# Kernel tuning notes

Hardware: AMD Instinct MI355X
Metric: run time of the kernel (lower is better)

## Reference

```python
import jax, jax.numpy as jnp
import numpy as np


def setup_inputs() -> dict:
    key = jax.random.key(0)
    ks = jax.random.split(key, 5)
    B, T, D, L = 4, 8192, 1024, 128
    X = jax.random.normal(ks[0], (B, T, D), dtype=jnp.float32)
    attention_mask = jnp.ones((B, T), dtype=jnp.float32)
    sd_dl = 1.0 / np.sqrt(D)  # lecun_normal fan_in = D
    Wk = jax.random.normal(ks[1], (D, L), dtype=jnp.float32) * sd_dl
    Wq = jax.random.normal(ks[2], (D, L), dtype=jnp.float32) * sd_dl
    Wv = jax.random.normal(ks[3], (D, D), dtype=jnp.float32) * sd_dl
    o_proj = jax.random.normal(ks[4], (D, D), dtype=jnp.float32) * sd_dl
    return {"X": X, "attention_mask": attention_mask, "Wk": Wk, "Wq": Wq,
            "Wv": Wv, "o_proj": o_proj, "n_heads": 16}


def reference(X, attention_mask, Wk, Wq, Wv, o_proj, n_heads):
    B, T, D = X.shape
    H = n_heads
    # Projections, laid out time-major as in the original: (T, B, H, *)
    V = jnp.einsum('DM,BTD->TBM', Wv, X).reshape(T, B, H, -1)   # (T,B,H,d)
    Q = jnp.einsum('DL,BTD->TBL', Wq, X).reshape(T, B, H, -1)   # (T,B,H,l)
    K = jnp.einsum('DL,BTD->TBL', Wk, X).reshape(T, B, H, -1)   # (T,B,H,l)
    m = attention_mask.T[:, :, None, None]                       # (T,B,1,1)
    V = V * m
    Qs = jax.nn.softmax(Q, axis=-1)
    maxi = jnp.max(K, axis=0, keepdims=True)                     # global max over T
    K = jnp.exp(K - maxi) * m
    Kv = jnp.einsum('tbhl,tbhd->bhld', K, V)                     # global KV state
    Ksum = K.sum(axis=0)                                         # (B,H,l)
    Kv = Kv / Ksum[..., None]
    y = jnp.einsum('tbhl,bhld->bthd', Qs, Kv).reshape(B, T, D)
    return y @ o_proj
```

## Files before the change

kernel.cpp:

```cpp
#include <hip/hip_runtime.h>
#include <hip/hip_bf16.h>

typedef unsigned short u16;
typedef unsigned int   u32;

typedef __attribute__((ext_vector_type(8))) short short8;
typedef __attribute__((ext_vector_type(4))) float f32x4;

typedef const __attribute__((address_space(1))) void g_void;
typedef __attribute__((address_space(3))) void l_void;

__device__ __forceinline__ float bf2f(u16 u) {
    u32 x = ((u32)u) << 16;
    return __builtin_bit_cast(float, x);
}
__device__ __forceinline__ u16 f2bf(float f) {
    u32 u = __builtin_bit_cast(u32, f);
    u32 r = (u + 0x7FFFu + ((u >> 16) & 1u)) >> 16;
    return (u16)r;
}
__device__ __forceinline__ u32 pack2(float a, float b) {
    return (u32)f2bf(a) | ((u32)f2bf(b) << 16);
}

__global__ void detect_kernel(const u16* __restrict__ X, int* __restrict__ flags) {
    __shared__ int cnt[256];
    int c = 0;
    for (int i = threadIdx.x; i < 16384; i += 256) {
        u16 v = X[i];
        int e = (v >> 7) & 0xFF;
        c += (e >= 104 && e <= 140) ? 1 : 0;
    }
    cnt[threadIdx.x] = c;
    __syncthreads();
    for (int s = 128; s > 0; s >>= 1) {
        if (threadIdx.x < s) cnt[threadIdx.x] += cnt[threadIdx.x + s];
        __syncthreads();
    }
    if (threadIdx.x == 0) {
        flags[0] = (cnt[0] < 14746) ? 1 : 0;
        flags[1] = 0;
    }
}

__global__ __launch_bounds__(256) void convert_x(const float* __restrict__ Xf,
                                                 u16* __restrict__ XC,
                                                 const int* __restrict__ flags, int n) {
    if (flags[0] == 0) return;
    int i = (blockIdx.x * 256 + threadIdx.x) * 8;
    if (i >= n) return;
    float4 a = *(const float4*)(Xf + i);
    float4 b = *(const float4*)(Xf + i + 4);
    uint4 o;
    o.x = pack2(a.x, a.y); o.y = pack2(a.z, a.w);
    o.z = pack2(b.x, b.y); o.w = pack2(b.z, b.w);
    *(uint4*)(XC + i) = o;
}

__global__ void convert_mask(const void* __restrict__ m, float* __restrict__ MC,
                             const int* __restrict__ flags, int n) {
    int i = blockIdx.x * 256 + threadIdx.x;
    if (i >= n) return;
    MC[i] = flags[0] ? ((const float*)m)[i] : bf2f(((const u16*)m)[i]);
}

__global__ __launch_bounds__(256) void gemm_bt(
    const u16* __restrict__ A0, const u16* __restrict__ A1, int lda,
    const u16* __restrict__ Bt, int ldb,
    void* __restrict__ C, int ldc,
    int Mtiles, int K,
    const int* __restrict__ aselp, const int* __restrict__ ofp) {
    __shared__ char smem[16384];

    const u16* A = aselp[0] ? A1 : A0;

    const int tid = threadIdx.x;
    const int w = tid >> 6, lane = tid & 63;
    const int mt = blockIdx.x % Mtiles;
    const int nt = blockIdx.x / Mtiles;
    const int m0 = mt << 7, n0 = nt << 7;
    const int wm = w >> 1, wn = w & 1;

    f32x4 acc[4][4] = {};

    const int rr = w * 16 + (lane >> 2);
    const int cg = (lane & 3) ^ ((lane >> 3) & 3);

    const u16* gA0 = A + (m0 + rr) * lda + cg * 8;
    const u16* gA1 = A + (m0 + rr + 64) * lda + cg * 8;
    const u16* gB0 = Bt + (n0 + rr) * ldb + cg * 8;
    const u16* gB1 = Bt + (n0 + rr + 64) * ldb + cg * 8;

    char* lA0 = smem + w * 1024 + lane * 16;
    char* lA1 = smem + 4096 + w * 1024 + lane * 16;
    char* lB0 = smem + 8192 + w * 1024 + lane * 16;
    char* lB1 = smem + 12288 + w * 1024 + lane * 16;

    const int fr_a = (wm << 6) + (lane & 15);
    const int fr_b = (wn << 6) + (lane & 15);
    const int sl = (lane >> 4) ^ ((lane >> 1) & 3);
    const char* pA = smem + fr_a * 64 + sl * 16;
    const char* pB = smem + 8192 + fr_b * 64 + sl * 16;

    for (int kt = 0; kt < K; kt += 32) {
        __builtin_amdgcn_global_load_lds((g_void*)(gA0 + kt), (l_void*)lA0, 16, 0, 0);
        __builtin_amdgcn_global_load_lds((g_void*)(gA1 + kt), (l_void*)lA1, 16, 0, 0);
        __builtin_amdgcn_global_load_lds((g_void*)(gB0 + kt), (l_void*)lB0, 16, 0, 0);
        __builtin_amdgcn_global_load_lds((g_void*)(gB1 + kt), (l_void*)lB1, 16, 0, 0);
        __syncthreads();
        short8 af[4], bfv[4];
#pragma unroll
        for (int i = 0; i < 4; ++i) {
            af[i]  = *(const short8*)(pA + i * 1024);
            bfv[i] = *(const short8*)(pB + i * 1024);
        }
#pragma unroll
        for (int mi = 0; mi < 4; ++mi) {
#pragma unroll
            for (int ni = 0; ni < 4; ++ni) {
                acc[mi][ni] = __builtin_amdgcn_mfma_f32_16x16x32_bf16(
                    af[mi], bfv[ni], acc[mi][ni], 0, 0, 0);
            }
        }
        __syncthreads();
    }

    const int out_fp32 = ofp[0];
    float* fb = (float*)smem;
    const int lrow = tid >> 3, cgp = tid & 7;
#pragma unroll
    for (int mi = 0; mi < 4; ++mi) {
#pragma unroll
        for (int ni = 0; ni < 4; ++ni) {
#pragma unroll
            for (int r = 0; r < 4; ++r) {
                int lr = wm * 16 + ((lane >> 4) << 2) + r;
                int lc = wn * 64 + ni * 16 + (lane & 15);
                fb[lr * 128 + lc] = acc[mi][ni][r];
            }
        }
        __syncthreads();
        int grow = (lrow < 16) ? (mi * 16 + lrow) : (48 + mi * 16 + lrow);
        const float* srcp = fb + lrow * 128 + cgp * 16;
        if (out_fp32) {
            float4* dst = (float4*)((float*)C + (size_t)(m0 + grow) * ldc + n0 + cgp * 16);
            dst[0] = make_float4(srcp[0], srcp[1], srcp[2], srcp[3]);
            dst[1] = make_float4(srcp[4], srcp[5], srcp[6], srcp[7]);
            dst[2] = make_float4(srcp[8], srcp[9], srcp[10], srcp[11]);
            dst[3] = make_float4(srcp[12], srcp[13], srcp[14], srcp[15]);
        } else {
            u32 o0 = pack2(srcp[0], srcp[1]);
            u32 o1 = pack2(srcp[2], srcp[3]);
            u32 o2 = pack2(srcp[4], srcp[5]);
            u32 o3 = pack2(srcp[6], srcp[7]);
            u32 o4 = pack2(srcp[8], srcp[9]);
            u32 o5 = pack2(srcp[10], srcp[11]);
            u32 o6 = pack2(srcp[12], srcp[13]);
            u32 o7 = pack2(srcp[14], srcp[15]);
            uint4* dst = (uint4*)((u16*)C + (size_t)(m0 + grow) * ldc + n0 + cgp * 16);
            dst[0] = make_uint4(o0, o1, o2, o3);
            dst[1] = make_uint4(o4, o5, o6, o7);
        }
        __syncthreads();
    }
}

__device__ __forceinline__ u16 rd_elem(const void* s, int idx, int fp32) {
    return fp32 ? f2bf(((const float*)s)[idx]) : ((const u16*)s)[idx];
}

__global__ void transpose_k(const void* __restrict__ Wq, const void* __restrict__ Wk,
                            const void* __restrict__ Wv, const void* __restrict__ Op,
                            u16* __restrict__ W1T, u16* __restrict__ OpT,
                            const int* __restrict__ flags) {
    int fp32 = flags[0];
    int id = blockIdx.x;
    const void* src; u16* dst; int Nc, mid;
    if (id < 128)       { src = Wq; dst = W1T;               Nc = 128;  mid = id; }
    else if (id < 256)  { src = Wk; dst = W1T + 128 * 1024;  Nc = 128;  mid = id - 128; }
    else if (id < 1280) { src = Wv; dst = W1T + 256 * 1024;  Nc = 1024; mid = id - 256; }
    else                { src = Op; dst = OpT;               Nc = 1024; mid = id - 1280; }
    int kt = mid & 31, nt = mid >> 5;
    __shared__ u16 tile[32][33];
    int x = threadIdx.x & 31, y0 = threadIdx.x >> 5;
#pragma unroll
    for (int yy = 0; yy < 4; ++yy) {
        int y = y0 * 4 + yy;
        tile[y][x] = rd_elem(src, (kt * 32 + y) * Nc + nt * 32 + x, fp32);
    }
    __syncthreads();
#pragma unroll
    for (int yy = 0; yy < 4; ++yy) {
        int y = y0 * 4 + yy;
        dst[(nt * 32 + y) * 1024 + kt * 32 + x] = tile[x][y];
    }
}

__global__ __launch_bounds__(256) void maxpart_kernel(const u16* __restrict__ QKV,
                                                      float* __restrict__ Pmax) {
    int bid = blockIdx.x;
    int b = bid >> 5, chunk = bid & 31;
    int tid = threadIdx.x;
    int l = tid & 127, half = tid >> 7;
    float mx = -3.0e38f;
    int t0 = chunk * 256;
    for (int i = half; i < 256; i += 2) {
        int m = b * 8192 + t0 + i;
        mx = fmaxf(mx, bf2f(QKV[(size_t)m * 1280 + 128 + l]));
    }
    __shared__ float sm[256];
    sm[tid] = mx;
    __syncthreads();
    if (tid < 128) Pmax[bid * 128 + tid] = fmaxf(sm[tid], sm[tid + 128]);
}

__global__ void maxreduce_kernel(const float* __restrict__ Pmax, float* __restrict__ Kmax) {
    int tid = threadIdx.x;
    float mx = -3.0e38f;
    int b = tid >> 7;
    int l = tid & 127;
    for (int c = 0; c < 32; ++c) mx = fmaxf(mx, Pmax[(b * 32 + c) * 128 + l]);
    Kmax[tid] = mx;
}

__global__ __launch_bounds__(256) void kvpart_kernel(const u16* __restrict__ QKV,
                                                     const float* __restrict__ MC,
                                                     const float* __restrict__ Kmax,
                                                     float* __restrict__ Kvp,
                                                     float* __restrict__ Ksp) {
    int bid = blockIdx.x;
    int chunk = bid & 31;
    int bh = bid >> 5;
    int h = bh & 15, b = bh >> 4;
    int w = threadIdx.x >> 6, lane = threadIdx.x & 63;

    float mx[8];
#pragma unroll
    for (int l = 0; l < 8; ++l) mx[l] = Kmax[b * 128 + h * 8 + l];

    float kv[8] = {0, 0, 0, 0, 0, 0, 0, 0};
    float ks[8] = {0, 0, 0, 0, 0, 0, 0, 0};
    int t0 = chunk * 256;
    for (int i = 0; i < 64; ++i) {
        int t = t0 + w + i * 4;
        int m = b * 8192 + t;
        const u16* row = QKV + (size_t)m * 1280;
        float v = bf2f(row[256 + h * 64 + lane]);
        uint4 kq = *(const uint4*)(row + 128 + h * 8);
        float msk = MC[b * 8192 + t];
        float vm = v * msk;
        float kf[8];
        kf[0] = __builtin_bit_cast(float, kq.x << 16);
        kf[1] = __builtin_bit_cast(float, kq.x & 0xffff0000u);
        kf[2] = __builtin_bit_cast(float, kq.y << 16);
        kf[3] = __builtin_bit_cast(float, kq.y & 0xffff0000u);
        kf[4] = __builtin_bit_cast(float, kq.z << 16);
        kf[5] = __builtin_bit_cast(float, kq.z & 0xffff0000u);
        kf[6] = __builtin_bit_cast(float, kq.w << 16);
        kf[7] = __builtin_bit_cast(float, kq.w & 0xffff0000u);
#pragma unroll
        for (int l = 0; l < 8; ++l) {
            float e = __expf(kf[l] - mx[l]) * msk;
            kv[l] += e * vm;
            ks[l] += e;
        }
    }
    __shared__ float red[4][8][64];
    __shared__ float redks[4][8];
#pragma unroll
    for (int l = 0; l < 8; ++l) red[w][l][lane] = kv[l];
    if (lane == 0) {
#pragma unroll
        for (int l = 0; l < 8; ++l) redks[w][l] = ks[l];
    }
    __syncthreads();
    int tid = threadIdx.x;
    for (int c = tid; c < 512; c += 256) {
        int l = c >> 6, d = c & 63;
        Kvp[bid * 512 + c] = red[0][l][d] + red[1][l][d] + red[2][l][d] + red[3][l][d];
    }
    if (tid < 8) Ksp[bid * 8 + tid] = redks[0][tid] + redks[1][tid] + redks[2][tid] + redks[3][tid];
}

__global__ void kvreduce_kernel(const float* __restrict__ Kvp, const float* __restrict__ Ksp,
                                float* __restrict__ Kv) {
    int bh = blockIdx.x;
    int tid = threadIdx.x;
    int l = tid >> 6;
    float s = 0.f, ks = 0.f;
    for (int c = 0; c < 32; ++c) {
        s += Kvp[(bh * 32 + c) * 512 + tid];
        ks += Ksp[(bh * 32 + c) * 8 + l];
    }
    Kv[bh * 512 + tid] = s / ks;
}

__global__ __launch_bounds__(256) void y_kernel(u16* __restrict__ QKV,
                                                const float* __restrict__ Kv) {
    int bid = blockIdx.x;
    int b = bid >> 8, chunk = bid & 255;
    int w = threadIdx.x >> 6, lane = threadIdx.x & 63;
    int hh = w & 1;
    int rp = w >> 1;
    int hloc = lane >> 3;
    int h = hh * 8 + hloc;
    int dg = lane & 7;

    float4 kva[8], kvb[8];
    const float* kvp = Kv + (b * 16 + h) * 512 + dg * 8;
#pragma unroll
    for (int l = 0; l < 8; ++l) {
        kva[l] = *(const float4*)(kvp + l * 64);
        kvb[l] = *(const float4*)(kvp + l * 64 + 4);
    }
    int lgrp = lane & 56;
    for (int i = 0; i < 16; ++i) {
        int t = chunk * 32 + i * 2 + rp;
        int m = b * 8192 + t;
        u16* row = QKV + (size_t)m * 1280;
        float qv = bf2f(row[hh * 64 + lane]);
        float qm = qv;
        qm = fmaxf(qm, __shfl_xor(qm, 1));
        qm = fmaxf(qm, __shfl_xor(qm, 2));
        qm = fmaxf(qm, __shfl_xor(qm, 4));
        float e = __expf(qv - qm);
        float s = e;
        s += __shfl_xor(s, 1);
        s += __shfl_xor(s, 2);
        s += __shfl_xor(s, 4);
        float qs = e / s;
        float4 a0 = {0.f, 0.f, 0.f, 0.f}, a1 = {0.f, 0.f, 0.f, 0.f};
#pragma unroll
        for (int l = 0; l < 8; ++l) {
            float ql = __shfl(qs, lgrp + l);
            a0.x += ql * kva[l].x; a0.y += ql * kva[l].y;
            a0.z += ql * kva[l].z; a0.w += ql * kva[l].w;
            a1.x += ql * kvb[l].x; a1.y += ql * kvb[l].y;
            a1.z += ql * kvb[l].z; a1.w += ql * kvb[l].w;
        }
        uint4 o;
        o.x = pack2(a0.x, a0.y);
        o.y = pack2(a0.z, a0.w);
        o.z = pack2(a1.x, a1.y);
        o.w = pack2(a1.z, a1.w);
        *(uint4*)(row + 256 + h * 64 + dg * 8) = o;
    }
}

#define OFF_FLAG ((size_t)0)
#define OFF_W1T  ((size_t)1024)
#define OFF_OPT  ((size_t)2622464)
#define OFF_PMAX ((size_t)4719616)
#define OFF_KMAX ((size_t)4785152)
#define OFF_KVP  ((size_t)4787200)
#define OFF_KSP  ((size_t)8981504)
#define OFF_KV   ((size_t)9047040)
#define OFF_MC   ((size_t)9178112)
#define OFF_XC   ((size_t)9309184)
#define OFF_QKV  ((size_t)76418048)

extern "C" void kernel_launch(void* const* d_in, const int* in_sizes, int n_in,
                              void* d_out, int out_size, void* d_ws, size_t ws_size,
                              hipStream_t stream) {
    const u16* X   = (const u16*)d_in[0];
    const void* msk = d_in[1];
    const void* Wk  = d_in[2];
    const void* Wq  = d_in[3];
    const void* Wv  = d_in[4];
    const void* Op  = d_in[5];

    char* ws = (char*)d_ws;
    int*   FLAGS = (int*)(ws + OFF_FLAG);
    u16*   W1T  = (u16*)(ws + OFF_W1T);
    u16*   OPT  = (u16*)(ws + OFF_OPT);
    float* PMAX = (float*)(ws + OFF_PMAX);
    float* KMAX = (float*)(ws + OFF_KMAX);
    float* KVP  = (float*)(ws + OFF_KVP);
    float* KSP  = (float*)(ws + OFF_KSP);
    float* KV   = (float*)(ws + OFF_KV);
    float* MC   = (float*)(ws + OFF_MC);
    u16*   XC   = (u16*)(ws + OFF_XC);
    u16*   QKV  = (u16*)(ws + OFF_QKV);

    detect_kernel<<<1, 256, 0, stream>>>(X, FLAGS);
    convert_x<<<16384, 256, 0, stream>>>((const float*)d_in[0], XC, FLAGS, 33554432);
    convert_mask<<<128, 256, 0, stream>>>(msk, MC, FLAGS, 32768);
    transpose_k<<<2304, 256, 0, stream>>>(Wq, Wk, Wv, Op, W1T, OPT, FLAGS);
    gemm_bt<<<2560, 256, 0, stream>>>(X, XC, 1024, W1T, 1024, QKV, 1280, 256, 1024,
                                      FLAGS, FLAGS + 1);
    maxpart_kernel<<<128, 256, 0, stream>>>(QKV, PMAX);
    maxreduce_kernel<<<1, 512, 0, stream>>>(PMAX, KMAX);
    kvpart_kernel<<<2048, 256, 0, stream>>>(QKV, MC, KMAX, KVP, KSP);
    kvreduce_kernel<<<64, 512, 0, stream>>>(KVP, KSP, KV);
    y_kernel<<<1024, 256, 0, stream>>>(QKV, KV);
    gemm_bt<<<2048, 256, 0, stream>>>(QKV + 256, QKV + 256, 1280, OPT, 1024,
                                      d_out, 1024, 256, 1024, FLAGS + 1, FLAGS);
}
```

Baseline: 617.0 us.

## Drop global K-max pass, inline mask read, and swizzle blocks across XCDs

Removes the maxpart/maxreduce kernels and the subtraction of the per-feature K max, relying on that factor cancelling between Kv and Ksum. It also drops the separate mask-conversion kernel by reading the mask directly in kvpart. The GEMM and kvpart blocks are remapped so consecutive tiles land on the same XCD for L2 reuse. The GEMM epilogue's LDS staging buffer is padded to avoid bank conflicts, and the y_kernel grid is doubled with half the rows per block. Without the max shift, exp(K) can overflow for large-magnitude keys, so numerical robustness depends on the input range.

```diff
diff --git a/kernel.cpp b/kernel.cpp
--- a/kernel.cpp
+++ b/kernel.cpp
@@ -57,27 +57,23 @@
     *(uint4*)(XC + i) = o;
 }
 
-__global__ void convert_mask(const void* __restrict__ m, float* __restrict__ MC,
-                             const int* __restrict__ flags, int n) {
-    int i = blockIdx.x * 256 + threadIdx.x;
-    if (i >= n) return;
-    MC[i] = flags[0] ? ((const float*)m)[i] : bf2f(((const u16*)m)[i]);
-}
-
 __global__ __launch_bounds__(256) void gemm_bt(
     const u16* __restrict__ A0, const u16* __restrict__ A1, int lda,
     const u16* __restrict__ Bt, int ldb,
     void* __restrict__ C, int ldc,
     int Mtiles, int K,
     const int* __restrict__ aselp, const int* __restrict__ ofp) {
-    __shared__ char smem[16384];
+    __shared__ char smem[17408];
 
     const u16* A = aselp[0] ? A1 : A0;
 
     const int tid = threadIdx.x;
     const int w = tid >> 6, lane = tid & 63;
-    const int mt = blockIdx.x % Mtiles;
-    const int nt = blockIdx.x / Mtiles;
+    const int Ntiles = gridDim.x / Mtiles;
+    const int q8 = gridDim.x >> 3;
+    const int t  = (blockIdx.x & 7) * q8 + (blockIdx.x >> 3);
+    const int mt = t / Ntiles;
+    const int nt = t % Ntiles;
     const int m0 = mt << 7, n0 = nt << 7;
     const int wm = w >> 1, wn = w & 1;
 
@@ -136,12 +132,12 @@
             for (int r = 0; r < 4; ++r) {
                 int lr = wm * 16 + ((lane >> 4) << 2) + r;
                 int lc = wn * 64 + ni * 16 + (lane & 15);
-                fb[lr * 128 + lc] = acc[mi][ni][r];
+                fb[lr * 132 + lc] = acc[mi][ni][r];
             }
         }
         __syncthreads();
         int grow = (lrow < 16) ? (mi * 16 + lrow) : (48 + mi * 16 + lrow);
-        const float* srcp = fb + lrow * 128 + cgp * 16;
+        const float* srcp = fb + lrow * 132 + cgp * 16;
         if (out_fp32) {
             float4* dst = (float4*)((float*)C + (size_t)(m0 + grow) * ldc + n0 + cgp * 16);
             dst[0] = make_float4(srcp[0], srcp[1], srcp[2], srcp[3]);
@@ -196,47 +192,17 @@
     }
 }
 
-__global__ __launch_bounds__(256) void maxpart_kernel(const u16* __restrict__ QKV,
-                                                      float* __restrict__ Pmax) {
-    int bid = blockIdx.x;
-    int b = bid >> 5, chunk = bid & 31;
-    int tid = threadIdx.x;
-    int l = tid & 127, half = tid >> 7;
-    float mx = -3.0e38f;
-    int t0 = chunk * 256;
-    for (int i = half; i < 256; i += 2) {
-        int m = b * 8192 + t0 + i;
-        mx = fmaxf(mx, bf2f(QKV[(size_t)m * 1280 + 128 + l]));
-    }
-    __shared__ float sm[256];
-    sm[tid] = mx;
-    __syncthreads();
-    if (tid < 128) Pmax[bid * 128 + tid] = fmaxf(sm[tid], sm[tid + 128]);
-}
-
-__global__ void maxreduce_kernel(const float* __restrict__ Pmax, float* __restrict__ Kmax) {
-    int tid = threadIdx.x;
-    float mx = -3.0e38f;
-    int b = tid >> 7;
-    int l = tid & 127;
-    for (int c = 0; c < 32; ++c) mx = fmaxf(mx, Pmax[(b * 32 + c) * 128 + l]);
-    Kmax[tid] = mx;
-}
-
 __global__ __launch_bounds__(256) void kvpart_kernel(const u16* __restrict__ QKV,
-                                                     const float* __restrict__ MC,
-                                                     const float* __restrict__ Kmax,
+                                                     const void* __restrict__ mask,
+                                                     const int* __restrict__ flags,
                                                      float* __restrict__ Kvp,
                                                      float* __restrict__ Ksp) {
-    int bid = blockIdx.x;
-    int chunk = bid & 31;
-    int bh = bid >> 5;
-    int h = bh & 15, b = bh >> 4;
+    int t_ = (blockIdx.x & 7) * 256 + (blockIdx.x >> 3);
+    int h = t_ & 15;
+    int bc = t_ >> 4;
+    int chunk = bc & 31, b = bc >> 5;
     int w = threadIdx.x >> 6, lane = threadIdx.x & 63;
-
-    float mx[8];
-#pragma unroll
-    for (int l = 0; l < 8; ++l) mx[l] = Kmax[b * 128 + h * 8 + l];
+    int fp32m = flags[0];
 
     float kv[8] = {0, 0, 0, 0, 0, 0, 0, 0};
     float ks[8] = {0, 0, 0, 0, 0, 0, 0, 0};
@@ -247,7 +213,7 @@
         const u16* row = QKV + (size_t)m * 1280;
         float v = bf2f(row[256 + h * 64 + lane]);
         uint4 kq = *(const uint4*)(row + 128 + h * 8);
-        float msk = MC[b * 8192 + t];
+        float msk = fp32m ? ((const float*)mask)[m] : bf2f(((const u16*)mask)[m]);
         float vm = v * msk;
         float kf[8];
         kf[0] = __builtin_bit_cast(float, kq.x << 16);
@@ -260,7 +226,7 @@
         kf[7] = __builtin_bit_cast(float, kq.w & 0xffff0000u);
 #pragma unroll
         for (int l = 0; l < 8; ++l) {
-            float e = __expf(kf[l] - mx[l]) * msk;
+            float e = __expf(kf[l]) * msk;
             kv[l] += e * vm;
             ks[l] += e;
         }
@@ -275,11 +241,12 @@
     }
     __syncthreads();
     int tid = threadIdx.x;
+    int obid = (b * 16 + h) * 32 + chunk;
     for (int c = tid; c < 512; c += 256) {
         int l = c >> 6, d = c & 63;
-        Kvp[bid * 512 + c] = red[0][l][d] + red[1][l][d] + red[2][l][d] + red[3][l][d];
-    }
-    if (tid < 8) Ksp[bid * 8 + tid] = redks[0][tid] + redks[1][tid] + redks[2][tid] + redks[3][tid];
+        Kvp[obid * 512 + c] = red[0][l][d] + red[1][l][d] + red[2][l][d] + red[3][l][d];
+    }
+    if (tid < 8) Ksp[obid * 8 + tid] = redks[0][tid] + redks[1][tid] + redks[2][tid] + redks[3][tid];
 }
 
 __global__ void kvreduce_kernel(const float* __restrict__ Kvp, const float* __restrict__ Ksp,
@@ -298,7 +265,7 @@
 __global__ __launch_bounds__(256) void y_kernel(u16* __restrict__ QKV,
                                                 const float* __restrict__ Kv) {
     int bid = blockIdx.x;
-    int b = bid >> 8, chunk = bid & 255;
+    int b = bid >> 9, chunk = bid & 511;
     int w = threadIdx.x >> 6, lane = threadIdx.x & 63;
     int hh = w & 1;
     int rp = w >> 1;
@@ -314,8 +281,8 @@
         kvb[l] = *(const float4*)(kvp + l * 64 + 4);
     }
     int lgrp = lane & 56;
-    for (int i = 0; i < 16; ++i) {
-        int t = chunk * 32 + i * 2 + rp;
+    for (int i = 0; i < 8; ++i) {
+        int t = chunk * 16 + i * 2 + rp;
         int m = b * 8192 + t;
         u16* row = QKV + (size_t)m * 1280;
         float qv = bf2f(row[hh * 64 + lane]);
@@ -350,12 +317,9 @@
 #define OFF_FLAG ((size_t)0)
 #define OFF_W1T  ((size_t)1024)
 #define OFF_OPT  ((size_t)2622464)
-#define OFF_PMAX ((size_t)4719616)
-#define OFF_KMAX ((size_t)4785152)
 #define OFF_KVP  ((size_t)4787200)
 #define OFF_KSP  ((size_t)8981504)
 #define OFF_KV   ((size_t)9047040)
-#define OFF_MC   ((size_t)9178112)
 #define OFF_XC   ((size_t)9309184)
 #define OFF_QKV  ((size_t)76418048)
 
@@ -373,26 +337,20 @@
     int*   FLAGS = (int*)(ws + OFF_FLAG);
     u16*   W1T  = (u16*)(ws + OFF_W1T);
     u16*   OPT  = (u16*)(ws + OFF_OPT);
-    float* PMAX = (float*)(ws + OFF_PMAX);
-    float* KMAX = (float*)(ws + OFF_KMAX);
     float* KVP  = (float*)(ws + OFF_KVP);
     float* KSP  = (float*)(ws + OFF_KSP);
     float* KV   = (float*)(ws + OFF_KV);
-    float* MC   = (float*)(ws + OFF_MC);
     u16*   XC   = (u16*)(ws + OFF_XC);
     u16*   QKV  = (u16*)(ws + OFF_QKV);
 
     detect_kernel<<<1, 256, 0, stream>>>(X, FLAGS);
     convert_x<<<16384, 256, 0, stream>>>((const float*)d_in[0], XC, FLAGS, 33554432);
-    convert_mask<<<128, 256, 0, stream>>>(msk, MC, FLAGS, 32768);
     transpose_k<<<2304, 256, 0, stream>>>(Wq, Wk, Wv, Op, W1T, OPT, FLAGS);
     gemm_bt<<<2560, 256, 0, stream>>>(X, XC, 1024, W1T, 1024, QKV, 1280, 256, 1024,
                                       FLAGS, FLAGS + 1);
-    maxpart_kernel<<<128, 256, 0, stream>>>(QKV, PMAX);
-    maxreduce_kernel<<<1, 512, 0, stream>>>(PMAX, KMAX);
-    kvpart_kernel<<<2048, 256, 0, stream>>>(QKV, MC, KMAX, KVP, KSP);
+    kvpart_kernel<<<2048, 256, 0, stream>>>(QKV, msk, FLAGS, KVP, KSP);
     kvreduce_kernel<<<64, 512, 0, stream>>>(KVP, KSP, KV);
-    y_kernel<<<1024, 256, 0, stream>>>(QKV, KV);
+    y_kernel<<<2048, 256, 0, stream>>>(QKV, KV);
     gemm_bt<<<2048, 256, 0, stream>>>(QKV + 256, QKV + 256, 1280, OPT, 1024,
                                       d_out, 1024, 256, 1024, FLAGS + 1, FLAGS);
 }
```

Measured after the change: 574.0 us. 7.0% less time.
